# Kernel tuning notes

Measured on AMD Instinct MI355X. Metric: run time of the kernel, lower is better.

Reference implementation:

```python
import jax, jax.numpy as jnp
import numpy as np

K = 3          # pooling factor (init k)
H_OUT = 8      # number of bilinear heads
H_DIM = 512    # hidden dim after pooling
BN_EPS = 1e-5
NEG_INF = -jnp.inf


def setup_inputs() -> dict:
    key = jax.random.key(0)
    ks = jax.random.split(key, 8)
    b, vn, qn, vd, qd = 16, 256, 256, 512, 768
    hk = H_DIM * K
    return {
        "v": jax.random.normal(ks[0], (b, vn, vd), jnp.float32),
        "q": jax.random.normal(ks[1], (b, qn, qd), jnp.float32),
        "Wv": jax.random.normal(ks[2], (hk, vd), jnp.float32) * 0.05,
        "bv": jax.random.normal(ks[3], (hk,), jnp.float32) * 0.05,
        "Wq": jax.random.normal(ks[4], (hk, qd), jnp.float32) * 0.05,
        "bq": jax.random.normal(ks[5], (hk,), jnp.float32) * 0.05,
        "h_mat": jax.random.normal(ks[6], (1, H_OUT, 1, hk), jnp.float32),
        "h_bias": jax.random.normal(ks[7], (1, H_OUT, 1, 1), jnp.float32),
        "bn_gamma": jnp.ones((H_DIM,), jnp.float32),
        "bn_beta": jnp.zeros((H_DIM,), jnp.float32),
    }


def _forward(v, q, Wv, bv, Wq, bq, h_mat, h_bias, bn_gamma, bn_beta):
    # FCNet (eval mode: dropout is identity; weight_norm folded into W)
    v_ = jax.nn.relu(jnp.einsum("bvd,kd->bvk", v, Wv) + bv)   # [b, vn, h_dim*k]
    q_ = jax.nn.relu(jnp.einsum("bqd,kd->bqk", q, Wq) + bq)   # [b, qn, h_dim*k]

    # Bilinear attention maps: [b, h_out, vn, qn]
    att = jnp.einsum("xhyk,bvk,bqk->bhvq", h_mat, v_, q_) + h_bias

    # v_mask / q_mask (all-zero token rows masked to -inf)
    v_zero = jnp.sum(jnp.abs(v), axis=2) == 0                  # [b, vn]
    q_zero = jnp.sum(jnp.abs(q), axis=2) == 0                  # [b, qn]
    att = jnp.where(v_zero[:, None, :, None], NEG_INF, att)
    att = jnp.where(q_zero[:, None, None, :], NEG_INF, att)

    # Fused per-head attention pooling, summed over heads (original Python loop)
    fused = jnp.einsum("bhvq,bqk->bhvk", att, q_)
    logits_k = jnp.einsum("bvk,bhvk->bk", v_, fused)           # [b, h_dim*k]

    # AvgPool1d(k, stride=k) * k  == sum over groups of k
    b = logits_k.shape[0]
    logits = logits_k.reshape(b, H_DIM, K).sum(axis=2)         # [b, h_dim]

    # BatchNorm1d (training-mode batch statistics, biased variance)
    mu = logits.mean(axis=0)
    var = logits.var(axis=0)
    logits = (logits - mu) * jax.lax.rsqrt(var + BN_EPS) * bn_gamma + bn_beta
    return logits, att


def reference(v, q, Wv, bv, Wq, bq, h_mat, h_bias, bn_gamma, bn_beta):
    return _forward(v, q, Wv, bv, Wq, bq, h_mat, h_bias, bn_gamma, bn_beta)
```

## Files before the change

### kernel.cpp

```cpp
#include <hip/hip_runtime.h>
#include <math.h>

#define BB    16
#define VN    256
#define QN    256
#define VD    512
#define QD    768
#define HK    1536
#define HDIM  512

typedef _Float16 half8 __attribute__((ext_vector_type(8)));
typedef _Float16 half4 __attribute__((ext_vector_type(4)));
typedef float f32x4 __attribute__((ext_vector_type(4)));

__device__ __forceinline__ void lds_barrier() {
    asm volatile("s_waitcnt lgkmcnt(0)" ::: "memory");
    __builtin_amdgcn_s_barrier();
}

__global__ __launch_bounds__(256) void conv_all(
    const float* __restrict__ v, const float* __restrict__ q,
    _Float16* __restrict__ v16in, _Float16* __restrict__ q16in,
    float* __restrict__ vz, float* __restrict__ qz,
    const float* __restrict__ Wv, _Float16* __restrict__ Wv16,
    const float* __restrict__ Wq, _Float16* __restrict__ Wq16,
    const float* __restrict__ hm, _Float16* __restrict__ hs16) {
    int g = blockIdx.x;
    int t = threadIdx.x;
    if (g < 2048) {
        int which = g >> 10;
        int gb = g & 1023;
        const float* src = which ? q : v;
        _Float16* dst = which ? q16in : v16in;
        float* outz = which ? qz : vz;
        int D = which ? QD : VD;
        int w = t >> 6, ln = t & 63;
        int row = gb * 4 + w;
        const float* p = src + (size_t)row * D;
        _Float16* d = dst + (size_t)row * D;
        float s = 0.f;
        for (int c = ln * 4; c < D; c += 256) {
            float4 x = *(const float4*)(p + c);
            s += fabsf(x.x) + fabsf(x.y) + fabsf(x.z) + fabsf(x.w);
            half4 hh = {(_Float16)x.x, (_Float16)x.y, (_Float16)x.z, (_Float16)x.w};
            *(half4*)(d + c) = hh;
        }
        for (int off = 32; off > 0; off >>= 1) s += __shfl_down(s, off);
        if (ln == 0) outz[row] = (s == 0.f) ? 1.f : 0.f;
        return;
    }
    if (g < 3968) {
        int isq = (g >= 2816);
        int gb = isq ? (g - 2816) : (g - 2048);
        const float* src = isq ? Wq : Wv;
        _Float16* dst = isq ? Wq16 : Wv16;
        int n4 = isq ? (HK * QD / 4) : (HK * VD / 4);
        int i = gb * 256 + t;
        if (i < n4) {
            float4 x = ((const float4*)src)[i];
            half4 h = {(_Float16)x.x, (_Float16)x.y, (_Float16)x.z, (_Float16)x.w};
            ((half4*)dst)[i] = h;
        }
        return;
    }
    {
        int k = (g - 3968) * 256 + t;
        if (k >= HK) return;
        float s = 0.f;
#pragma unroll
        for (int h = 0; h < 8; ++h) {
            float x = hm[h * HK + k];
            s += x;
            hs16[h * HK + k] = (_Float16)x;
        }
        hs16[8 * HK + k] = (_Float16)s;
    }
}

__global__ __launch_bounds__(256, 2) void proj128(
    const _Float16* __restrict__ v16in, const _Float16* __restrict__ Wv16,
    const float* __restrict__ bv, _Float16* __restrict__ v16,
    const _Float16* __restrict__ q16in, const _Float16* __restrict__ Wq16,
    const float* __restrict__ bq, _Float16* __restrict__ q16) {
    __shared__ _Float16 As[128 * 64];
    __shared__ _Float16 Bs[128 * 64];
    int lin = blockIdx.x;
    int gg = (lin & 7) * 96 + (lin >> 3);
    int z = gg / 384;
    int r = gg - z * 384;
    int m0 = (r / 12) * 128, n0 = (r % 12) * 128;
    const _Float16* Ain = z ? q16in : v16in;
    const _Float16* W16 = z ? Wq16 : Wv16;
    const float* bias = z ? bq : bv;
    _Float16* C16 = z ? q16 : v16;
    int K = z ? QD : VD;
    int t = threadIdx.x;
    int w = t >> 6, ln = t & 63, quad = ln >> 4, r16 = ln & 15;
    int wi = w & 1, wj = w >> 1;
    int arow = t >> 3, aseg = t & 7;
    int sg = (aseg ^ (arow & 7)) * 8;
    const _Float16* ApG = Ain + (size_t)(m0 + arow) * K + aseg * 8;
    const _Float16* BpG = W16 + (size_t)(n0 + arow) * K + aseg * 8;
    half8 ra[4], rb[4];
#pragma unroll
    for (int c = 0; c < 4; ++c) {
        ra[c] = *(const half8*)(ApG + (size_t)c * 32 * K);
        rb[c] = *(const half8*)(BpG + (size_t)c * 32 * K);
    }
    f32x4 acc[4][4] = {};
    for (int k0 = 0; k0 < K; k0 += 64) {
        lds_barrier();
#pragma unroll
        for (int c = 0; c < 4; ++c) {
            *(half8*)&As[(c * 32 + arow) * 64 + sg] = ra[c];
            *(half8*)&Bs[(c * 32 + arow) * 64 + sg] = rb[c];
        }
        lds_barrier();
        if (k0 + 64 < K) {
#pragma unroll
            for (int c = 0; c < 4; ++c) {
                ra[c] = *(const half8*)(ApG + (size_t)c * 32 * K + k0 + 64);
                rb[c] = *(const half8*)(BpG + (size_t)c * 32 * K + k0 + 64);
            }
        }
#pragma unroll
        for (int kc = 0; kc < 2; ++kc) {
            half8 af[4], bf[4];
#pragma unroll
            for (int fi = 0; fi < 4; ++fi) {
                int rl = wi * 64 + fi * 16 + r16;
                af[fi] = *(const half8*)&As[rl * 64 + ((kc * 4 + quad) ^ (rl & 7)) * 8];
            }
#pragma unroll
            for (int fj = 0; fj < 4; ++fj) {
                int rl = wj * 64 + fj * 16 + r16;
                bf[fj] = *(const half8*)&Bs[rl * 64 + ((kc * 4 + quad) ^ (rl & 7)) * 8];
            }
#pragma unroll
            for (int fi = 0; fi < 4; ++fi)
#pragma unroll
                for (int fj = 0; fj < 4; ++fj)
                    acc[fi][fj] = __builtin_amdgcn_mfma_f32_16x16x32_f16(
                        af[fi], bf[fj], acc[fi][fj], 0, 0, 0);
        }
    }
#pragma unroll
    for (int fi = 0; fi < 4; ++fi) {
#pragma unroll
        for (int r2 = 0; r2 < 4; ++r2) {
            int m = m0 + wi * 64 + fi * 16 + quad * 4 + r2;
#pragma unroll
            for (int fj = 0; fj < 4; ++fj) {
                int n = n0 + wj * 64 + fj * 16 + r16;
                float x = acc[fi][fj][r2] + bias[n];
                C16[(size_t)m * HK + n] = (_Float16)fmaxf(x, 0.f);
            }
        }
    }
}

__global__ __launch_bounds__(256, 2) void att_2h(
    const _Float16* __restrict__ v16, const _Float16* __restrict__ q16,
    const _Float16* __restrict__ hs16, const float* __restrict__ hb,
    const float* __restrict__ vz, const float* __restrict__ qz,
    float* __restrict__ att_out, _Float16* __restrict__ A16) {
    __shared__ _Float16 As[2][32 * 64];
    __shared__ _Float16 Bs[2][64 * 64];
    __shared__ _Float16 Hl[8 * HK];
    __shared__ float Red[3][32 * 64];
    int lin = blockIdx.x;
    int swz = ((lin & 7) << 6) | (lin >> 3);
    int jb = swz & 3, ib = (swz >> 2) & 7, b = swz >> 5;
    int i0 = ib * 32, j0 = jb * 64;
    int t = threadIdx.x;
    int hg = t >> 6, ln = t & 63, quad = ln >> 4, r16 = ln & 15;
    int h0 = hg * 2;
    int arow = t >> 3, aseg = t & 7;
    int sg = (aseg ^ (arow & 7)) * 8;
    for (int u = t * 8; u < 8 * HK; u += 256 * 8)
        *(half8*)&Hl[u] = *(const half8*)(hs16 + u);
    const _Float16* ApG = v16 + (size_t)b * VN * HK + (size_t)(i0 + arow) * HK + aseg * 8;
    const _Float16* BpG = q16 + (size_t)b * QN * HK + (size_t)(j0 + arow) * HK + aseg * 8;
    half8 ra, rb[2];
    ra    = *(const half8*)(ApG);
    rb[0] = *(const half8*)(BpG);
    rb[1] = *(const half8*)(BpG + (size_t)32 * HK);
    *(half8*)&As[0][arow * 64 + sg] = ra;
    *(half8*)&Bs[0][arow * 64 + sg] = rb[0];
    *(half8*)&Bs[0][(arow + 32) * 64 + sg] = rb[1];
    ra    = *(const half8*)(ApG + 64);
    rb[0] = *(const half8*)(BpG + 64);
    rb[1] = *(const half8*)(BpG + (size_t)32 * HK + 64);
    f32x4 acc[2][2][4] = {};
    for (int it = 0; it < 24; ++it) {
        lds_barrier();
        int cur = it & 1;
        const _Float16* Ac = As[cur];
        const _Float16* Bc = Bs[cur];
        if (it + 1 < 24) {
            int nxt = cur ^ 1;
            *(half8*)&As[nxt][arow * 64 + sg] = ra;
            *(half8*)&Bs[nxt][arow * 64 + sg] = rb[0];
            *(half8*)&Bs[nxt][(arow + 32) * 64 + sg] = rb[1];
        }
        if (it + 2 < 24) {
            int kn = (it + 2) * 64;
            ra    = *(const half8*)(ApG + kn);
            rb[0] = *(const half8*)(BpG + kn);
            rb[1] = *(const half8*)(BpG + (size_t)32 * HK + kn);
        }
        int kb = it * 64;
#pragma unroll
        for (int kc = 0; kc < 2; ++kc) {
            half8 af[2], bf[4];
#pragma unroll
            for (int fi = 0; fi < 2; ++fi) {
                int rl = fi * 16 + r16;
                af[fi] = *(const half8*)&Ac[rl * 64 + ((kc * 4 + quad) ^ (rl & 7)) * 8];
            }
#pragma unroll
            for (int fj = 0; fj < 4; ++fj) {
                int rl = fj * 16 + r16;
                bf[fj] = *(const half8*)&Bc[rl * 64 + ((kc * 4 + quad) ^ (rl & 7)) * 8];
            }
#pragma unroll
            for (int hh = 0; hh < 2; ++hh) {
                half8 hmv = *(const half8*)&Hl[(h0 + hh) * HK + kb + (kc * 4 + quad) * 8];
#pragma unroll
                for (int fi = 0; fi < 2; ++fi) {
                    half8 am = af[fi] * hmv;
#pragma unroll
                    for (int fj = 0; fj < 4; ++fj)
                        acc[hh][fi][fj] = __builtin_amdgcn_mfma_f32_16x16x32_f16(
                            am, bf[fj], acc[hh][fi][fj], 0, 0, 0);
                }
            }
        }
    }
    float s[2][4][4];
#pragma unroll
    for (int fi = 0; fi < 2; ++fi)
#pragma unroll
        for (int fj = 0; fj < 4; ++fj)
#pragma unroll
            for (int r = 0; r < 4; ++r)
                s[fi][fj][r] = acc[0][fi][fj][r] + acc[1][fi][fj][r];
    float hbv[2];
#pragma unroll
    for (int hh = 0; hh < 2; ++hh) hbv[hh] = hb[h0 + hh];
    float hbsum = 0.f;
#pragma unroll
    for (int h = 0; h < 8; ++h) hbsum += hb[h];
    float qm[4];
#pragma unroll
    for (int fj = 0; fj < 4; ++fj) qm[fj] = qz[b * QN + j0 + fj * 16 + r16];
    float* outb = att_out + (size_t)b * 8 * VN * QN;
#pragma unroll
    for (int fi = 0; fi < 2; ++fi) {
#pragma unroll
        for (int r = 0; r < 4; ++r) {
            int i = i0 + fi * 16 + quad * 4 + r;
            float vm = vz[b * VN + i];
#pragma unroll
            for (int fj = 0; fj < 4; ++fj) {
                int j = j0 + fj * 16 + r16;
                bool msk = (vm != 0.f) || (qm[fj] != 0.f);
#pragma unroll
                for (int hh = 0; hh < 2; ++hh) {
                    float x = acc[hh][fi][fj][r] + hbv[hh];
                    if (msk) x = -INFINITY;
                    outb[(size_t)(h0 + hh) * VN * QN + (size_t)i * QN + j] = x;
                }
            }
        }
    }
    if (hg) {
#pragma unroll
        for (int fi = 0; fi < 2; ++fi)
#pragma unroll
            for (int fj = 0; fj < 4; ++fj)
#pragma unroll
                for (int r = 0; r < 4; ++r)
                    Red[hg - 1][(fi * 16 + quad * 4 + r) * 64 + fj * 16 + r16] =
                        s[fi][fj][r];
    }
    __syncthreads();
    if (!hg) {
        _Float16* Ab = A16 + (size_t)b * VN * QN;
#pragma unroll
        for (int fi = 0; fi < 2; ++fi) {
#pragma unroll
            for (int r = 0; r < 4; ++r) {
                int i = i0 + fi * 16 + quad * 4 + r;
                float vm = vz[b * VN + i];
#pragma unroll
                for (int fj = 0; fj < 4; ++fj) {
                    int j = j0 + fj * 16 + r16;
                    int ri = (fi * 16 + quad * 4 + r) * 64 + fj * 16 + r16;
                    float tot = s[fi][fj][r] + Red[0][ri] + Red[1][ri] + Red[2][ri] + hbsum;
                    if (vm != 0.f || qm[fj] != 0.f) tot = -INFINITY;
                    Ab[(size_t)i * QN + j] = (_Float16)tot;
                }
            }
        }
    }
}

__global__ __launch_bounds__(256) void t_lk_ft(
    const _Float16* __restrict__ A16, const _Float16* __restrict__ q16,
    const _Float16* __restrict__ v16, float* __restrict__ lk) {
    __shared__ _Float16 As[256 * 32];
    __shared__ _Float16 Bs[64 * 32];
    __shared__ float red[16][64];
    int b = blockIdx.y;
    int k0 = blockIdx.x * 64;
    int t = threadIdx.x;
    int w = t >> 6, ln = t & 63, quad = ln >> 4, r16 = ln & 15;
    const _Float16* Ab = A16 + (size_t)b * VN * QN;
    const _Float16* Qb = q16 + (size_t)b * QN * HK;
    int ar = t >> 2, aseg = t & 3;
    int tj = t & 31, tk = t >> 5;
    f32x4 acc[4][4] = {};
    for (int j0 = 0; j0 < QN; j0 += 32) {
        half8 a0 = *(const half8*)(Ab + (size_t)(ar +   0) * QN + j0 + aseg * 8);
        half8 a1 = *(const half8*)(Ab + (size_t)(ar +  64) * QN + j0 + aseg * 8);
        half8 a2 = *(const half8*)(Ab + (size_t)(ar + 128) * QN + j0 + aseg * 8);
        half8 a3 = *(const half8*)(Ab + (size_t)(ar + 192) * QN + j0 + aseg * 8);
        half8 q8 = *(const half8*)(Qb + (size_t)(j0 + tj) * HK + k0 + tk * 8);
        __syncthreads();
        *(half8*)&As[(ar +   0) * 32 + aseg * 8] = a0;
        *(half8*)&As[(ar +  64) * 32 + aseg * 8] = a1;
        *(half8*)&As[(ar + 128) * 32 + aseg * 8] = a2;
        *(half8*)&As[(ar + 192) * 32 + aseg * 8] = a3;
#pragma unroll
        for (int e = 0; e < 8; ++e)
            Bs[(tk * 8 + e) * 32 + tj] = q8[e];
        __syncthreads();
        half8 af[4], bf[4];
#pragma unroll
        for (int fi = 0; fi < 4; ++fi)
            af[fi] = *(const half8*)&As[(w * 64 + fi * 16 + r16) * 32 + quad * 8];
#pragma unroll
        for (int fj = 0; fj < 4; ++fj)
            bf[fj] = *(const half8*)&Bs[(fj * 16 + r16) * 32 + quad * 8];
#pragma unroll
        for (int fi = 0; fi < 4; ++fi)
#pragma unroll
            for (int fj = 0; fj < 4; ++fj)
                acc[fi][fj] = __builtin_amdgcn_mfma_f32_16x16x32_f16(
                    af[fi], bf[fj], acc[fi][fj], 0, 0, 0);
    }
    const _Float16* Vb = v16 + (size_t)b * VN * HK;
    float part[4] = {0.f, 0.f, 0.f, 0.f};
#pragma unroll
    for (int fi = 0; fi < 4; ++fi) {
#pragma unroll
        for (int r = 0; r < 4; ++r) {
            int i = w * 64 + fi * 16 + quad * 4 + r;
#pragma unroll
            for (int fj = 0; fj < 4; ++fj) {
                float vv = (float)Vb[(size_t)i * HK + k0 + fj * 16 + r16];
                part[fj] += acc[fi][fj][r] * vv;
            }
        }
    }
#pragma unroll
    for (int fj = 0; fj < 4; ++fj)
        red[w * 4 + quad][fj * 16 + r16] = part[fj];
    __syncthreads();
    if (t < 64) {
        float s = 0.f;
#pragma unroll
        for (int g = 0; g < 16; ++g) s += red[g][t];
        lk[b * HK + k0 + t] = s;
    }
}

__global__ __launch_bounds__(256) void bn_kernel(
    const float* __restrict__ lk, const float* __restrict__ gamma,
    const float* __restrict__ beta, float* __restrict__ out) {
    int d = blockIdx.x * blockDim.x + threadIdx.x;
    if (d >= HDIM) return;
    float l[BB];
    float mu = 0.f;
#pragma unroll
    for (int b = 0; b < BB; ++b) {
        const float* p = lk + b * HK + 3 * d;
        float s = p[0] + p[1] + p[2];
        l[b] = s;
        mu += s;
    }
    mu *= (1.f / BB);
    float var = 0.f;
#pragma unroll
    for (int b = 0; b < BB; ++b) {
        float dd = l[b] - mu;
        var += dd * dd;
    }
    var *= (1.f / BB);
    float inv = rsqrtf(var + 1e-5f);
    float g = gamma[d], be = beta[d];
#pragma unroll
    for (int b = 0; b < BB; ++b)
        out[b * HDIM + d] = (l[b] - mu) * inv * g + be;
}

extern "C" void kernel_launch(void* const* d_in, const int* in_sizes, int n_in,
                              void* d_out, int out_size, void* d_ws, size_t ws_size,
                              hipStream_t stream) {
    const float* v  = (const float*)d_in[0];
    const float* q  = (const float*)d_in[1];
    const float* Wv = (const float*)d_in[2];
    const float* bv = (const float*)d_in[3];
    const float* Wq = (const float*)d_in[4];
    const float* bq = (const float*)d_in[5];
    const float* hm = (const float*)d_in[6];
    const float* hb = (const float*)d_in[7];
    const float* gamma = (const float*)d_in[8];
    const float* beta  = (const float*)d_in[9];

    float* out_logits = (float*)d_out;
    float* out_att    = out_logits + BB * HDIM;

    _Float16* h = (_Float16*)d_ws;
    _Float16* v16   = h;
    _Float16* q16   = v16 + (size_t)BB * VN * HK;
    _Float16* A16   = q16 + (size_t)BB * QN * HK;
    _Float16* v16in = A16 + (size_t)BB * VN * QN;
    _Float16* q16in = v16in + (size_t)BB * VN * VD;
    _Float16* Wv16  = q16in + (size_t)BB * QN * QD;
    _Float16* Wq16  = Wv16 + (size_t)HK * VD;
    _Float16* hs16  = Wq16 + (size_t)HK * QD;
    float* lk = (float*)(hs16 + 9 * HK + 8);
    float* vz = lk + BB * HK;
    float* qz = vz + BB * VN;

    conv_all<<<dim3(3974), 256, 0, stream>>>(
        v, q, v16in, q16in, vz, qz, Wv, Wv16, Wq, Wq16, hm, hs16);

    proj128<<<dim3(768), 256, 0, stream>>>(
        v16in, Wv16, bv, v16, q16in, Wq16, bq, q16);

    att_2h<<<dim3(512), 256, 0, stream>>>(
        v16, q16, hs16, hb, vz, qz, out_att, A16);

    t_lk_ft<<<dim3(HK / 64, BB), 256, 0, stream>>>(A16, q16, v16, lk);

    bn_kernel<<<dim3((HDIM + 255) / 256), 256, 0, stream>>>(lk, gamma, beta, out_logits);
}
```

Before: 169.1 us.

## Use direct global-to-LDS loads with 4-stage ring buffer in attention kernel

Replaces the register-staged double-buffered loads in the bilinear attention kernel with global_load_lds async copies into a 4-deep LDS ring, gating each iteration with vmcnt waits and a single barrier. The reduction scratch buffer now reuses the B tile storage instead of its own LDS allocation, which keeps LDS use manageable with the deeper ring. This is meant to remove the VGPR round trip and the ds_write instructions for tile staging and to overlap more memory latency. The risk is the extra barrier before the reduction and correctness of the swizzled per-lane LDS destination layout.

```diff
diff --git a/kernel.cpp b/kernel.cpp
--- a/kernel.cpp
+++ b/kernel.cpp
@@ -16,6 +16,12 @@
 __device__ __forceinline__ void lds_barrier() {
     asm volatile("s_waitcnt lgkmcnt(0)" ::: "memory");
     __builtin_amdgcn_s_barrier();
+}
+
+typedef const __attribute__((address_space(1))) void* gp1_t;
+typedef __attribute__((address_space(3))) void* lp3_t;
+__device__ __forceinline__ void gld16(const _Float16* g, _Float16* l) {
+    __builtin_amdgcn_global_load_lds((gp1_t)g, (lp3_t)l, 16, 0, 0);
 }
 
 __global__ __launch_bounds__(256) void conv_all(
@@ -159,15 +165,14 @@
     }
 }
 
-__global__ __launch_bounds__(256, 2) void att_2h(
+__global__ __launch_bounds__(256, 2) void att_gl(
     const _Float16* __restrict__ v16, const _Float16* __restrict__ q16,
     const _Float16* __restrict__ hs16, const float* __restrict__ hb,
     const float* __restrict__ vz, const float* __restrict__ qz,
     float* __restrict__ att_out, _Float16* __restrict__ A16) {
-    __shared__ _Float16 As[2][32 * 64];
-    __shared__ _Float16 Bs[2][64 * 64];
+    __shared__ _Float16 As[4][32 * 64];
+    __shared__ _Float16 Bs[4][64 * 64];
     __shared__ _Float16 Hl[8 * HK];
-    __shared__ float Red[3][32 * 64];
     int lin = blockIdx.x;
     int swz = ((lin & 7) << 6) | (lin >> 3);
     int jb = swz & 3, ib = (swz >> 2) & 7, b = swz >> 5;
@@ -175,40 +180,35 @@
     int t = threadIdx.x;
     int hg = t >> 6, ln = t & 63, quad = ln >> 4, r16 = ln & 15;
     int h0 = hg * 2;
-    int arow = t >> 3, aseg = t & 7;
-    int sg = (aseg ^ (arow & 7)) * 8;
+    int lrow = ln >> 3, lseg = ln & 7;
+    int lchunk = lseg ^ lrow;
+    const _Float16* Asrc = v16 + (size_t)b * VN * HK +
+                           (size_t)(i0 + hg * 8 + lrow) * HK + lchunk * 8;
+    const _Float16* Bsrc0 = q16 + (size_t)b * QN * HK +
+                            (size_t)(j0 + hg * 16 + lrow) * HK + lchunk * 8;
+    const _Float16* Bsrc1 = Bsrc0 + (size_t)8 * HK;
+#define STAGE(kt, bf_)                                            \
+    do {                                                          \
+        int kk = (kt) * 64;                                       \
+        gld16(Asrc + kk, &As[bf_][(hg * 8) * 64]);                \
+        gld16(Bsrc0 + kk, &Bs[bf_][(hg * 16) * 64]);              \
+        gld16(Bsrc1 + kk, &Bs[bf_][(hg * 16 + 8) * 64]);          \
+    } while (0)
+    STAGE(0, 0);
+    STAGE(1, 1);
     for (int u = t * 8; u < 8 * HK; u += 256 * 8)
         *(half8*)&Hl[u] = *(const half8*)(hs16 + u);
-    const _Float16* ApG = v16 + (size_t)b * VN * HK + (size_t)(i0 + arow) * HK + aseg * 8;
-    const _Float16* BpG = q16 + (size_t)b * QN * HK + (size_t)(j0 + arow) * HK + aseg * 8;
-    half8 ra, rb[2];
-    ra    = *(const half8*)(ApG);
-    rb[0] = *(const half8*)(BpG);
-    rb[1] = *(const half8*)(BpG + (size_t)32 * HK);
-    *(half8*)&As[0][arow * 64 + sg] = ra;
-    *(half8*)&Bs[0][arow * 64 + sg] = rb[0];
-    *(half8*)&Bs[0][(arow + 32) * 64 + sg] = rb[1];
-    ra    = *(const half8*)(ApG + 64);
-    rb[0] = *(const half8*)(BpG + 64);
-    rb[1] = *(const half8*)(BpG + (size_t)32 * HK + 64);
+    lds_barrier();
     f32x4 acc[2][2][4] = {};
     for (int it = 0; it < 24; ++it) {
-        lds_barrier();
-        int cur = it & 1;
+        if (it < 23) asm volatile("s_waitcnt vmcnt(3)" ::: "memory");
+        else         asm volatile("s_waitcnt vmcnt(0)" ::: "memory");
+        __builtin_amdgcn_sched_barrier(0);
+        __builtin_amdgcn_s_barrier();
+        int cur = it & 3;
+        if (it + 2 < 24) STAGE(it + 2, (it + 2) & 3);
         const _Float16* Ac = As[cur];
         const _Float16* Bc = Bs[cur];
-        if (it + 1 < 24) {
-            int nxt = cur ^ 1;
-            *(half8*)&As[nxt][arow * 64 + sg] = ra;
-            *(half8*)&Bs[nxt][arow * 64 + sg] = rb[0];
-            *(half8*)&Bs[nxt][(arow + 32) * 64 + sg] = rb[1];
-        }
-        if (it + 2 < 24) {
-            int kn = (it + 2) * 64;
-            ra    = *(const half8*)(ApG + kn);
-            rb[0] = *(const half8*)(BpG + kn);
-            rb[1] = *(const half8*)(BpG + (size_t)32 * HK + kn);
-        }
         int kb = it * 64;
 #pragma unroll
         for (int kc = 0; kc < 2; ++kc) {
@@ -237,6 +237,7 @@
             }
         }
     }
+#undef STAGE
     float s[2][4][4];
 #pragma unroll
     for (int fi = 0; fi < 2; ++fi)
@@ -274,6 +275,8 @@
             }
         }
     }
+    __syncthreads();
+    float* Red = (float*)&Bs[0][0];
     if (hg) {
 #pragma unroll
         for (int fi = 0; fi < 2; ++fi)
@@ -281,7 +284,7 @@
             for (int fj = 0; fj < 4; ++fj)
 #pragma unroll
                 for (int r = 0; r < 4; ++r)
-                    Red[hg - 1][(fi * 16 + quad * 4 + r) * 64 + fj * 16 + r16] =
+                    Red[(hg - 1) * 2048 + (fi * 16 + quad * 4 + r) * 64 + fj * 16 + r16] =
                         s[fi][fj][r];
     }
     __syncthreads();
@@ -297,7 +300,7 @@
                 for (int fj = 0; fj < 4; ++fj) {
                     int j = j0 + fj * 16 + r16;
                     int ri = (fi * 16 + quad * 4 + r) * 64 + fj * 16 + r16;
-                    float tot = s[fi][fj][r] + Red[0][ri] + Red[1][ri] + Red[2][ri] + hbsum;
+                    float tot = s[fi][fj][r] + Red[ri] + Red[2048 + ri] + Red[4096 + ri] + hbsum;
                     if (vm != 0.f || qm[fj] != 0.f) tot = -INFINITY;
                     Ab[(size_t)i * QN + j] = (_Float16)tot;
                 }
@@ -441,7 +444,7 @@
     proj128<<<dim3(768), 256, 0, stream>>>(
         v16in, Wv16, bv, v16, q16in, Wq16, bq, q16);
 
-    att_2h<<<dim3(512), 256, 0, stream>>>(
+    att_gl<<<dim3(512), 256, 0, stream>>>(
         v16, q16, hs16, hb, vz, qz, out_att, A16);
 
     t_lk_ft<<<dim3(HK / 64, BB), 256, 0, stream>>>(A16, q16, v16, lk);
```

Result: slower. 177.1 us (+4.8%).
